# Optimization experiments

Hardware: AMD Instinct MI355X
Metric: run time of the kernel (lower is better)

## Reference

```python
import jax, jax.numpy as jnp
import numpy as np

N = 8192
D = 512
EPS = 1e-12  # F.normalize default eps


def setup_inputs() -> dict:
    key = jax.random.key(0)
    k1, k2 = jax.random.split(key)
    cur = jax.random.normal(k1, (N, D), dtype=jnp.float32)
    # randn -> mixed-sign entries, so every row of (incidence_m > 0) is unique
    # (the only case where the original `incidence_m += head` shapes agree).
    incidence_m = jax.random.normal(k2, (N, N), dtype=jnp.float32)
    return {"cur": cur, "incidence_m": incidence_m}


def reference(cur, incidence_m):
    # construct_directed: dedup rows of (incidence_m > 0); with all rows unique,
    # each node is its own hyperedge leader and head == mask as float, row order
    # preserved. head is built from python ints in torch, hence non-differentiable.
    mask = incidence_m > 0
    head = jax.lax.stop_gradient(mask.astype(incidence_m.dtype))  # [N, N]
    # F.normalize(head, dim=-1): L2 per row with eps clamp
    head = head / jnp.maximum(
        jnp.sqrt(jnp.sum(head * head, axis=-1, keepdims=True)), EPS
    )
    inc = incidence_m + head                          # [N, N]
    edge_fea = inc @ cur                              # [N, D]
    edge_degree = jnp.sum(inc, axis=-1, keepdims=True)  # [N, 1]
    return edge_fea / edge_degree
```

## Files before the change

kernel.cpp:

```cpp
#include <hip/hip_runtime.h>
#include <stdint.h>


#define NROWS 8192
#define DDIM  512

typedef float f32x4 __attribute__((ext_vector_type(4)));
typedef short s16x8 __attribute__((ext_vector_type(8)));

__device__ __forceinline__ unsigned short f2bf(float f) {
  union { float f; unsigned int u; } c; c.f = f;
  unsigned int u = c.u;
  unsigned int r = u + 0x7FFFu + ((u >> 16) & 1u);
  return (unsigned short)(r >> 16);
}

__global__ __launch_bounds__(256) void stats_kernel(const float* __restrict__ inc,
                                                    float* __restrict__ invs,
                                                    float* __restrict__ rdeg) {
  int row = blockIdx.x;
  int tid = threadIdx.x;
  const float4* p = (const float4*)(inc + (size_t)row * NROWS);
  double s = 0.0;
  int c = 0;
#pragma unroll
  for (int i = 0; i < 8; ++i) {
    float4 v = p[i * 256 + tid];
    s += (double)v.x + (double)v.y + (double)v.z + (double)v.w;
    c += (v.x > 0.f) + (v.y > 0.f) + (v.z > 0.f) + (v.w > 0.f);
  }
  for (int off = 32; off > 0; off >>= 1) {
    s += __shfl_down(s, off);
    c += __shfl_down(c, off);
  }
  __shared__ double sw[4];
  __shared__ int cw[4];
  int lane = tid & 63, wv = tid >> 6;
  if (lane == 0) { sw[wv] = s; cw[wv] = c; }
  __syncthreads();
  if (tid == 0) {
    double S = sw[0] + sw[1] + sw[2] + sw[3];
    int C = cw[0] + cw[1] + cw[2] + cw[3];
    double sq = sqrt((double)C);
    invs[row] = (C > 0) ? (float)(1.0 / sq) : 0.0f;
    rdeg[row] = (float)(1.0 / (S + sq));
  }
}

__global__ __launch_bounds__(256) void bprep_kernel(const float* __restrict__ cur,
                                                    unsigned char* __restrict__ bws) {
  int idx = blockIdx.x * 256 + threadIdx.x;
  int n = idx & 511;
  int kg9 = idx >> 9;
  int kt = kg9 >> 3;
  int kg = kg9 & 7;
  int k0 = kt * 64 + kg * 8;
  union { unsigned short h[8]; uint4 q; } u;
#pragma unroll
  for (int e = 0; e < 8; ++e)
    u.h[e] = f2bf(cur[(size_t)(k0 + e) * DDIM + n]);
  int nt = n >> 8, nn = n & 255;
  size_t off = ((size_t)(nt * 128 + kt) << 15) + ((size_t)kg << 12) + ((size_t)nn << 4);
  *(uint4*)(bws + off) = u.q;
}


#define FENCE() __builtin_amdgcn_sched_barrier(0)
#define BARRIER() __builtin_amdgcn_s_barrier()
#define WAITVM2() asm volatile("s_waitcnt vmcnt(2) lgkmcnt(0)" ::: "memory")
#define WAITVM0() asm volatile("s_waitcnt vmcnt(0) lgkmcnt(0)" ::: "memory")

__global__ __launch_bounds__(512) void gemm_kernel(const float* __restrict__ inc,
                                                   const unsigned char* __restrict__ bws,
                                                   const float* __restrict__ invs,
                                                   const float* __restrict__ rdeg,
                                                   float* __restrict__ out) {
  __shared__ __align__(16) unsigned char smem[82176];
  unsigned char* const bBuf0 = smem;
  unsigned char* const bBuf1 = smem + 32768;
  unsigned char* const aBuf0 = smem + 65536;
  unsigned char* const aBuf1 = smem + 73728;
  float* const rdegS = (float*)(smem + 81920);

  const int tid = threadIdx.x;
  const int lane = tid & 63;
  const int wv = tid >> 6;
  const int nt = blockIdx.x;
  const int mt = blockIdx.y;
  const int brow = mt * 64;
  const int bcol = nt * 256;
  const int wr = wv >> 2, wc = wv & 3;

  if (tid < 64) rdegS[tid] = rdeg[brow + tid];

  const int sm = tid >> 3;
  const int sp = tid & 7;
  const float4* gAr = (const float4*)(inc + (size_t)(brow + sm) * NROWS) + sp * 2;
  const float invr = invs[brow + sm];
  const int aWr = (sp << 10) + ((sm ^ sp) << 4);

  const unsigned char* gB = bws + ((size_t)(nt * 128) << 15);
  const int gOffLane = (wv << 10) + (lane << 4);
  const int ldsWave = (wv << 10);

  int aOff[2][2], bOff[2][4];
#pragma unroll
  for (int kh = 0; kh < 2; ++kh) {
    int kg = kh * 4 + (lane >> 4);
#pragma unroll
    for (int g = 0; g < 2; ++g) {
      int r = wr * 32 + g * 16 + (lane & 15);
      aOff[kh][g] = (kg << 10) + ((r ^ kg) << 4);
    }
#pragma unroll
    for (int g = 0; g < 4; ++g)
      bOff[kh][g] = (kg << 12) + ((wc * 64 + g * 16 + (lane & 15)) << 4);
  }

  f32x4 acc[2][4];
#pragma unroll
  for (int a = 0; a < 2; ++a)
#pragma unroll
    for (int b = 0; b < 4; ++b)
      acc[a][b] = (f32x4){0.f, 0.f, 0.f, 0.f};

  float4 x0, x1, y0, y1;

#define ISSUE_A(d0, d1, KT) do { d0 = gAr[(KT) * 16]; d1 = gAr[(KT) * 16 + 1]; } while (0)

#define ISSUE_B(KT, BDST) do {                                                            \
    const unsigned char* _g = gB + ((size_t)(KT) << 15);                                  \
    _Pragma("unroll")                                                                     \
    for (int _s = 0; _s < 4; ++_s)                                                        \
      __builtin_amdgcn_global_load_lds(                                                   \
          (const __attribute__((address_space(1))) unsigned int*)(_g + (_s << 13) + gOffLane), \
          (__attribute__((address_space(3))) unsigned int*)((BDST) + (_s << 13) + ldsWave),    \
          16, 0, 0);                                                                      \
  } while (0)

#define XFORM(s0, s1, ADST) do {                                                          \
    uint4 _w;                                                                             \
    _w.x = (unsigned int)f2bf(s0.x + (s0.x > 0.f ? invr : 0.f)) |                         \
           ((unsigned int)f2bf(s0.y + (s0.y > 0.f ? invr : 0.f)) << 16);                  \
    _w.y = (unsigned int)f2bf(s0.z + (s0.z > 0.f ? invr : 0.f)) |                         \
           ((unsigned int)f2bf(s0.w + (s0.w > 0.f ? invr : 0.f)) << 16);                  \
    _w.z = (unsigned int)f2bf(s1.x + (s1.x > 0.f ? invr : 0.f)) |                         \
           ((unsigned int)f2bf(s1.y + (s1.y > 0.f ? invr : 0.f)) << 16);                  \
    _w.w = (unsigned int)f2bf(s1.z + (s1.z > 0.f ? invr : 0.f)) |                         \
           ((unsigned int)f2bf(s1.w + (s1.w > 0.f ? invr : 0.f)) << 16);                  \
    *(uint4*)((ADST) + aWr) = _w;                                                         \
  } while (0)

#define MFMA_TILE(AC, BC) do {                                                            \
    __builtin_amdgcn_s_setprio(1);                                                        \
    _Pragma("unroll")                                                                     \
    for (int kh = 0; kh < 2; ++kh) {                                                      \
      s16x8 af[2], bfr[4];                                                                \
      _Pragma("unroll")                                                                   \
      for (int g = 0; g < 2; ++g) af[g] = *(const s16x8*)((AC) + aOff[kh][g]);            \
      _Pragma("unroll")                                                                   \
      for (int g = 0; g < 4; ++g) bfr[g] = *(const s16x8*)((BC) + bOff[kh][g]);           \
      _Pragma("unroll")                                                                   \
      for (int rg = 0; rg < 2; ++rg)                                                      \
        _Pragma("unroll")                                                                 \
        for (int cg = 0; cg < 4; ++cg)                                                    \
          acc[rg][cg] = __builtin_amdgcn_mfma_f32_16x16x32_bf16(af[rg], bfr[cg],          \
                                                                acc[rg][cg], 0, 0, 0);   \
    }                                                                                     \
    __builtin_amdgcn_s_setprio(0);                                                        \
  } while (0)

  ISSUE_A(x0, x1, 0);
  ISSUE_B(0, bBuf0);
  ISSUE_A(y0, y1, 1);
  XFORM(x0, x1, aBuf0);
  FENCE();
  WAITVM2();
  FENCE();
  BARRIER();
  FENCE();
  ISSUE_B(1, bBuf1);

  for (int kt = 0; kt < 126; kt += 2) {
    ISSUE_A(x0, x1, kt + 2);
    MFMA_TILE(aBuf0, bBuf0);
    XFORM(y0, y1, aBuf1);
    FENCE();
    WAITVM2();
    FENCE();
    BARRIER();
    FENCE();
    ISSUE_B(kt + 2, bBuf0);
    ISSUE_A(y0, y1, kt + 3);
    MFMA_TILE(aBuf1, bBuf1);
    XFORM(x0, x1, aBuf0);
    FENCE();
    WAITVM2();
    FENCE();
    BARRIER();
    FENCE();
    ISSUE_B(kt + 3, bBuf1);
  }

  MFMA_TILE(aBuf0, bBuf0);
  XFORM(y0, y1, aBuf1);
  FENCE();
  WAITVM0();
  FENCE();
  BARRIER();
  FENCE();
  MFMA_TILE(aBuf1, bBuf1);

#pragma unroll
  for (int rg = 0; rg < 2; ++rg) {
    int rb = wr * 32 + rg * 16 + ((lane >> 4) << 2);
#pragma unroll
    for (int cg = 0; cg < 4; ++cg) {
      int col = bcol + wc * 64 + cg * 16 + (lane & 15);
#pragma unroll
      for (int r = 0; r < 4; ++r) {
        int rl = rb + r;
        out[(size_t)(brow + rl) * DDIM + col] = acc[rg][cg][r] * rdegS[rl];
      }
    }
  }
#undef ISSUE_A
#undef ISSUE_B
#undef XFORM
#undef MFMA_TILE
}

extern "C" void kernel_launch(void* const* d_in, const int* in_sizes, int n_in,
                              void* d_out, int out_size, void* d_ws, size_t ws_size,
                              hipStream_t stream) {
  const float* cur = (const float*)d_in[0];
  const float* incm = (const float*)d_in[1];
  float* out = (float*)d_out;
  unsigned char* ws = (unsigned char*)d_ws;
  float* invs = (float*)ws;
  float* rdeg = (float*)(ws + 32768);
  unsigned char* bws = ws + 65536;

  hipLaunchKernelGGL(stats_kernel, dim3(NROWS), dim3(256), 0, stream, incm, invs, rdeg);
  hipLaunchKernelGGL(bprep_kernel, dim3((NROWS / 64) * 8 * DDIM / 256), dim3(256), 0, stream,
                     cur, bws);
  hipLaunchKernelGGL(gemm_kernel, dim3(2, 128), dim3(512), 0, stream, incm, bws, invs, rdeg, out);
}
```

Baseline: 182.1 us.

## Fuse row stats into GEMM and split mask term into second MFMA accumulator

Removes the separate stats pass over the 256MB incidence matrix. Row sums and positive counts are now computed inside the GEMM while A tiles are loaded. Because the per-row normalisation scale is not known until the end, the mask contribution is accumulated in a second set of MFMAs on a bit-derived 0/1 bf16 fragment and scaled in the epilogue. The M tile is halved to 32 rows to fit the doubled accumulators, which doubles the grid and re-reads B more often. The MFMA work per output doubles, and the mask is derived from bf16-rounded values, so values that round to zero could be classified differently from the fp32 reference.

```diff
diff --git a/kernel.cpp b/kernel.cpp
--- a/kernel.cpp
+++ b/kernel.cpp
@@ -7,6 +7,7 @@
 
 typedef float f32x4 __attribute__((ext_vector_type(4)));
 typedef short s16x8 __attribute__((ext_vector_type(8)));
+typedef unsigned int u32x4 __attribute__((ext_vector_type(4)));
 
 __device__ __forceinline__ unsigned short f2bf(float f) {
   union { float f; unsigned int u; } c; c.f = f;
@@ -15,36 +16,17 @@
   return (unsigned short)(r >> 16);
 }
 
-__global__ __launch_bounds__(256) void stats_kernel(const float* __restrict__ inc,
-                                                    float* __restrict__ invs,
-                                                    float* __restrict__ rdeg) {
-  int row = blockIdx.x;
-  int tid = threadIdx.x;
-  const float4* p = (const float4*)(inc + (size_t)row * NROWS);
-  double s = 0.0;
-  int c = 0;
-#pragma unroll
-  for (int i = 0; i < 8; ++i) {
-    float4 v = p[i * 256 + tid];
-    s += (double)v.x + (double)v.y + (double)v.z + (double)v.w;
-    c += (v.x > 0.f) + (v.y > 0.f) + (v.z > 0.f) + (v.w > 0.f);
-  }
-  for (int off = 32; off > 0; off >>= 1) {
-    s += __shfl_down(s, off);
-    c += __shfl_down(c, off);
-  }
-  __shared__ double sw[4];
-  __shared__ int cw[4];
-  int lane = tid & 63, wv = tid >> 6;
-  if (lane == 0) { sw[wv] = s; cw[wv] = c; }
-  __syncthreads();
-  if (tid == 0) {
-    double S = sw[0] + sw[1] + sw[2] + sw[3];
-    int C = cw[0] + cw[1] + cw[2] + cw[3];
-    double sq = sqrt((double)C);
-    invs[row] = (C > 0) ? (float)(1.0 / sq) : 0.0f;
-    rdeg[row] = (float)(1.0 / (S + sq));
-  }
+__device__ __forceinline__ s16x8 pos_mask_frag(s16x8 a) {
+  union { s16x8 s; u32x4 u; } in, out;
+  in.s = a;
+#pragma unroll
+  for (int i = 0; i < 4; ++i) {
+    unsigned int v = in.u[i];
+    unsigned int nz = ((v & 0x7FFF7FFFu) + 0x7FFF7FFFu) & 0x80008000u;
+    unsigned int pos = nz & ~v;
+    out.u[i] = (pos >> 15) * 0x3F80u;
+  }
+  return out.s;
 }
 
 __global__ __launch_bounds__(256) void bprep_kernel(const float* __restrict__ cur,
@@ -67,66 +49,64 @@
 
 #define FENCE() __builtin_amdgcn_sched_barrier(0)
 #define BARRIER() __builtin_amdgcn_s_barrier()
-#define WAITVM2() asm volatile("s_waitcnt vmcnt(2) lgkmcnt(0)" ::: "memory")
+#define WAITVM1() asm volatile("s_waitcnt vmcnt(1) lgkmcnt(0)" ::: "memory")
 #define WAITVM0() asm volatile("s_waitcnt vmcnt(0) lgkmcnt(0)" ::: "memory")
 
-__global__ __launch_bounds__(512) void gemm_kernel(const float* __restrict__ inc,
-                                                   const unsigned char* __restrict__ bws,
-                                                   const float* __restrict__ invs,
-                                                   const float* __restrict__ rdeg,
-                                                   float* __restrict__ out) {
-  __shared__ __align__(16) unsigned char smem[82176];
+__global__ __launch_bounds__(512, 4) void gemm_kernel(const float* __restrict__ inc,
+                                                      const unsigned char* __restrict__ bws,
+                                                      float* __restrict__ out) {
+  __shared__ __align__(16) unsigned char smem[74240];
   unsigned char* const bBuf0 = smem;
   unsigned char* const bBuf1 = smem + 32768;
   unsigned char* const aBuf0 = smem + 65536;
-  unsigned char* const aBuf1 = smem + 73728;
-  float* const rdegS = (float*)(smem + 81920);
+  unsigned char* const aBuf1 = smem + 69632;
+  float* const invsS = (float*)(smem + 73728);
+  float* const rdegS = invsS + 32;
 
   const int tid = threadIdx.x;
   const int lane = tid & 63;
   const int wv = tid >> 6;
   const int nt = blockIdx.x;
   const int mt = blockIdx.y;
-  const int brow = mt * 64;
+  const int brow = mt * 32;
   const int bcol = nt * 256;
-  const int wr = wv >> 2, wc = wv & 3;
-
-  if (tid < 64) rdegS[tid] = rdeg[brow + tid];
-
-  const int sm = tid >> 3;
-  const int sp = tid & 7;
-  const float4* gAr = (const float4*)(inc + (size_t)(brow + sm) * NROWS) + sp * 2;
-  const float invr = invs[brow + sm];
-  const int aWr = (sp << 10) + ((sm ^ sp) << 4);
+
+  const int sm = tid >> 4;
+  const int sp = tid & 15;
+  const int kgw = sp >> 1, half = sp & 1;
+  const float4* gAr = (const float4*)(inc + (size_t)(brow + sm) * NROWS) + sp;
+  const int aWr = (kgw << 9) + (((sm ^ kgw)) << 4) + (half << 3);
 
   const unsigned char* gB = bws + ((size_t)(nt * 128) << 15);
   const int gOffLane = (wv << 10) + (lane << 4);
   const int ldsWave = (wv << 10);
 
-  int aOff[2][2], bOff[2][4];
+  int aOff[2][2], bOff[2][2];
 #pragma unroll
   for (int kh = 0; kh < 2; ++kh) {
     int kg = kh * 4 + (lane >> 4);
 #pragma unroll
     for (int g = 0; g < 2; ++g) {
-      int r = wr * 32 + g * 16 + (lane & 15);
-      aOff[kh][g] = (kg << 10) + ((r ^ kg) << 4);
+      int r = g * 16 + (lane & 15);
+      aOff[kh][g] = (kg << 9) + ((r ^ kg) << 4);
+      bOff[kh][g] = (kg << 12) + ((wv * 32 + g * 16 + (lane & 15)) << 4);
     }
-#pragma unroll
-    for (int g = 0; g < 4; ++g)
-      bOff[kh][g] = (kg << 12) + ((wc * 64 + g * 16 + (lane & 15)) << 4);
-  }
-
-  f32x4 acc[2][4];
+  }
+
+  f32x4 acc1[2][2], acc2[2][2];
 #pragma unroll
   for (int a = 0; a < 2; ++a)
 #pragma unroll
-    for (int b = 0; b < 4; ++b)
-      acc[a][b] = (f32x4){0.f, 0.f, 0.f, 0.f};
-
-  float4 x0, x1, y0, y1;
-
-#define ISSUE_A(d0, d1, KT) do { d0 = gAr[(KT) * 16]; d1 = gAr[(KT) * 16 + 1]; } while (0)
+    for (int b = 0; b < 2; ++b) {
+      acc1[a][b] = (f32x4){0.f, 0.f, 0.f, 0.f};
+      acc2[a][b] = (f32x4){0.f, 0.f, 0.f, 0.f};
+    }
+
+  double s1d = 0.0;
+  int cnt = 0;
+  float4 x, y;
+
+#define ISSUE_A(d, KT) do { d = gAr[(KT) * 16]; } while (0)
 
 #define ISSUE_B(KT, BDST) do {                                                            \
     const unsigned char* _g = gB + ((size_t)(KT) << 15);                                  \
@@ -138,64 +118,67 @@
           16, 0, 0);                                                                      \
   } while (0)
 
-#define XFORM(s0, s1, ADST) do {                                                          \
-    uint4 _w;                                                                             \
-    _w.x = (unsigned int)f2bf(s0.x + (s0.x > 0.f ? invr : 0.f)) |                         \
-           ((unsigned int)f2bf(s0.y + (s0.y > 0.f ? invr : 0.f)) << 16);                  \
-    _w.y = (unsigned int)f2bf(s0.z + (s0.z > 0.f ? invr : 0.f)) |                         \
-           ((unsigned int)f2bf(s0.w + (s0.w > 0.f ? invr : 0.f)) << 16);                  \
-    _w.z = (unsigned int)f2bf(s1.x + (s1.x > 0.f ? invr : 0.f)) |                         \
-           ((unsigned int)f2bf(s1.y + (s1.y > 0.f ? invr : 0.f)) << 16);                  \
-    _w.w = (unsigned int)f2bf(s1.z + (s1.z > 0.f ? invr : 0.f)) |                         \
-           ((unsigned int)f2bf(s1.w + (s1.w > 0.f ? invr : 0.f)) << 16);                  \
-    *(uint4*)((ADST) + aWr) = _w;                                                         \
+#define XFORM(s0, ADST) do {                                                              \
+    s1d += (double)s0.x + (double)s0.y + (double)s0.z + (double)s0.w;                     \
+    cnt += (s0.x > 0.f) + (s0.y > 0.f) + (s0.z > 0.f) + (s0.w > 0.f);                     \
+    unsigned long long pk =                                                               \
+        (unsigned long long)f2bf(s0.x) |                                                  \
+        ((unsigned long long)f2bf(s0.y) << 16) |                                          \
+        ((unsigned long long)f2bf(s0.z) << 32) |                                          \
+        ((unsigned long long)f2bf(s0.w) << 48);                                           \
+    *(unsigned long long*)((ADST) + aWr) = pk;                                            \
   } while (0)
 
 #define MFMA_TILE(AC, BC) do {                                                            \
     __builtin_amdgcn_s_setprio(1);                                                        \
     _Pragma("unroll")                                                                     \
     for (int kh = 0; kh < 2; ++kh) {                                                      \
-      s16x8 af[2], bfr[4];                                                                \
+      s16x8 af[2], am[2], bfr[2];                                                         \
       _Pragma("unroll")                                                                   \
       for (int g = 0; g < 2; ++g) af[g] = *(const s16x8*)((AC) + aOff[kh][g]);            \
       _Pragma("unroll")                                                                   \
-      for (int g = 0; g < 4; ++g) bfr[g] = *(const s16x8*)((BC) + bOff[kh][g]);           \
+      for (int g = 0; g < 2; ++g) bfr[g] = *(const s16x8*)((BC) + bOff[kh][g]);           \
+      _Pragma("unroll")                                                                   \
+      for (int g = 0; g < 2; ++g) am[g] = pos_mask_frag(af[g]);                           \
       _Pragma("unroll")                                                                   \
       for (int rg = 0; rg < 2; ++rg)                                                      \
         _Pragma("unroll")                                                                 \
-        for (int cg = 0; cg < 4; ++cg)                                                    \
-          acc[rg][cg] = __builtin_amdgcn_mfma_f32_16x16x32_bf16(af[rg], bfr[cg],          \
-                                                                acc[rg][cg], 0, 0, 0);   \
+        for (int cg = 0; cg < 2; ++cg) {                                                  \
+          acc1[rg][cg] = __builtin_amdgcn_mfma_f32_16x16x32_bf16(af[rg], bfr[cg],         \
+                                                                 acc1[rg][cg], 0, 0, 0); \
+          acc2[rg][cg] = __builtin_amdgcn_mfma_f32_16x16x32_bf16(am[rg], bfr[cg],         \
+                                                                 acc2[rg][cg], 0, 0, 0); \
+        }                                                                                 \
     }                                                                                     \
     __builtin_amdgcn_s_setprio(0);                                                        \
   } while (0)
 
-  ISSUE_A(x0, x1, 0);
+  ISSUE_A(x, 0);
   ISSUE_B(0, bBuf0);
-  ISSUE_A(y0, y1, 1);
-  XFORM(x0, x1, aBuf0);
-  FENCE();
-  WAITVM2();
+  ISSUE_A(y, 1);
+  XFORM(x, aBuf0);
+  FENCE();
+  WAITVM1();
   FENCE();
   BARRIER();
   FENCE();
   ISSUE_B(1, bBuf1);
 
   for (int kt = 0; kt < 126; kt += 2) {
-    ISSUE_A(x0, x1, kt + 2);
+    ISSUE_A(x, kt + 2);
     MFMA_TILE(aBuf0, bBuf0);
-    XFORM(y0, y1, aBuf1);
-    FENCE();
-    WAITVM2();
+    XFORM(y, aBuf1);
+    FENCE();
+    WAITVM1();
     FENCE();
     BARRIER();
     FENCE();
     ISSUE_B(kt + 2, bBuf0);
-    ISSUE_A(y0, y1, kt + 3);
+    ISSUE_A(y, kt + 3);
     MFMA_TILE(aBuf1, bBuf1);
-    XFORM(x0, x1, aBuf0);
-    FENCE();
-    WAITVM2();
+    XFORM(x, aBuf0);
+    FENCE();
+    WAITVM1();
     FENCE();
     BARRIER();
     FENCE();
@@ -203,7 +186,7 @@
   }
 
   MFMA_TILE(aBuf0, bBuf0);
-  XFORM(y0, y1, aBuf1);
+  XFORM(y, aBuf1);
   FENCE();
   WAITVM0();
   FENCE();
@@ -212,15 +195,28 @@
   MFMA_TILE(aBuf1, bBuf1);
 
 #pragma unroll
+  for (int o = 1; o < 16; o <<= 1) {
+    s1d += __shfl_xor(s1d, o);
+    cnt += __shfl_xor(cnt, o);
+  }
+  if (sp == 0) {
+    double sq = sqrt((double)cnt);
+    invsS[sm] = (cnt > 0) ? (float)(1.0 / sq) : 0.0f;
+    rdegS[sm] = (float)(1.0 / (s1d + sq));
+  }
+  __syncthreads();
+
+#pragma unroll
   for (int rg = 0; rg < 2; ++rg) {
-    int rb = wr * 32 + rg * 16 + ((lane >> 4) << 2);
-#pragma unroll
-    for (int cg = 0; cg < 4; ++cg) {
-      int col = bcol + wc * 64 + cg * 16 + (lane & 15);
+    int rb = rg * 16 + ((lane >> 4) << 2);
+#pragma unroll
+    for (int cg = 0; cg < 2; ++cg) {
+      int col = bcol + wv * 32 + cg * 16 + (lane & 15);
 #pragma unroll
       for (int r = 0; r < 4; ++r) {
         int rl = rb + r;
-        out[(size_t)(brow + rl) * DDIM + col] = acc[rg][cg][r] * rdegS[rl];
+        out[(size_t)(brow + rl) * DDIM + col] =
+            (acc1[rg][cg][r] + invsS[rl] * acc2[rg][cg][r]) * rdegS[rl];
       }
     }
   }
@@ -236,13 +232,9 @@
   const float* cur = (const float*)d_in[0];
   const float* incm = (const float*)d_in[1];
   float* out = (float*)d_out;
-  unsigned char* ws = (unsigned char*)d_ws;
-  float* invs = (float*)ws;
-  float* rdeg = (float*)(ws + 32768);
-  unsigned char* bws = ws + 65536;
-
-  hipLaunchKernelGGL(stats_kernel, dim3(NROWS), dim3(256), 0, stream, incm, invs, rdeg);
-  hipLaunchKernelGGL(bprep_kernel, dim3((NROWS / 64) * 8 * DDIM / 256), dim3(256), 0, stream,
+  unsigned char* bws = (unsigned char*)d_ws;
+
+  hipLaunchKernelGGL(bprep_kernel, dim3((NROWS * DDIM / 8) / 256), dim3(256), 0, stream,
                      cur, bws);
-  hipLaunchKernelGGL(gemm_kernel, dim3(2, 128), dim3(512), 0, stream, incm, bws, invs, rdeg, out);
-}
+  hipLaunchKernelGGL(gemm_kernel, dim3(2, 256), dim3(512), 0, stream, incm, bws, out);
+}
```

Result: slower. 207.2 us (+13.8%).
